# Kernel tuning notes

Measured on AMD Instinct MI355X. Metric: run time of the kernel, lower is better.

## Reference

```python
import jax, jax.numpy as jnp
import numpy as np

N, G, NPG = 8192, 128, 64        # total nodes, graphs, nodes per graph
D_IN, H, D_OUT = 128, 128, 10
DEG = 16                          # avg degree -> E = N*DEG
K = int(NPG * 0.5)                # keep_ratio = 0.5 -> topk per graph


def setup_inputs() -> dict:
    key = jax.random.key(0)
    ks = jax.random.split(key, 20)
    E = N * DEG
    # within-graph random edges (graphs are contiguous blocks of NPG nodes)
    src = jax.random.randint(ks[0], (E,), 0, NPG)
    dst = jax.random.randint(ks[1], (E,), 0, NPG)
    offs = jnp.repeat(jnp.arange(G, dtype=jnp.int32) * NPG, NPG * DEG)
    edge_index = jnp.stack([src.astype(jnp.int32) + offs, dst.astype(jnp.int32) + offs])
    batch = jnp.repeat(jnp.arange(G, dtype=jnp.int32), NPG)
    x = jax.random.normal(ks[2], (N, D_IN), jnp.float32)

    def lin(k, i, o):
        return jax.random.normal(k, (i, o), jnp.float32) * (1.0 / np.sqrt(i))

    return {
        "x": x, "edge_index": edge_index, "batch": batch,
        "W1": lin(ks[3], D_IN, H), "b1": jnp.zeros((H,), jnp.float32),
        "W2": lin(ks[4], H, H),    "b2": jnp.zeros((H,), jnp.float32),
        "W3": lin(ks[5], H, H),    "b3": jnp.zeros((H,), jnp.float32),
        "Wa": lin(ks[6], 3 * H, 1), "ba": jnp.zeros((1,), jnp.float32),
        "M1": lin(ks[7], 6 * H, H),      "c1": jnp.zeros((H,), jnp.float32),
        "M2": lin(ks[8], H, H // 2),     "c2": jnp.zeros((H // 2,), jnp.float32),
        "M3": lin(ks[9], H // 2, D_OUT), "c3": jnp.zeros((D_OUT,), jnp.float32),
    }


def reference(x, edge_index, batch, W1, b1, W2, b2, W3, b3, Wa, ba,
              M1, c1, M2, c2, M3, c3):
    n = x.shape[0]
    # generate_adjacency: dense [N,N] from edge list (symmetrized)
    A = jnp.zeros((n, n), x.dtype).at[edge_index[0], edge_index[1]].set(1.0)
    A = jnp.maximum(A, A.T)
    # normalize_adjacency: D^{-1/2} (A + I) D^{-1/2}
    A = A + jnp.eye(n, dtype=x.dtype)
    dinv = jax.lax.rsqrt(A.sum(axis=1))
    A = A * dinv[:, None] * dinv[None, :]

    gcn = lambda X, W, b: A @ (X @ W) + b
    h1 = jax.nn.relu(gcn(x, W1, b1))
    h2 = jax.nn.relu(gcn(h1, W2, b2))
    h3 = jax.nn.relu(gcn(h2, W3, b3))
    feats = jnp.concatenate([h1, h2, h3], axis=1)          # [N, 3H]

    # SelfAttentionPooling: GCN attention score + tanh + per-graph topk
    score = jnp.tanh((A @ (feats @ Wa) + ba)[:, 0])        # [N]
    s = score.reshape(G, NPG)                              # [G, NPG]
    _, idx = jax.lax.top_k(s, K)                           # [G, K]
    fg = feats.reshape(G, NPG, 3 * H)
    sel = jnp.take_along_axis(fg, idx[..., None], axis=1)  # [G, K, 3H]
    ssel = jnp.take_along_axis(s, idx, axis=1)             # [G, K]
    masked = sel * ssel[..., None]

    # Readout: mean || max per graph -> [G, 6H]
    readout = jnp.concatenate([masked.mean(axis=1), masked.max(axis=1)], axis=1)

    # MLP (dropout inactive at inference)
    h = jax.nn.relu(readout @ M1 + c1)
    h = jax.nn.relu(h @ M2 + c2)
    return h @ M3 + c3                                     # [G, D_OUT]
```

## Files before the change

### kernel.cpp

```cpp
#include <hip/hip_runtime.h>


#define NGRAPH 128
#define EPG    1024
#define ETOT   131072
#define DIM    128
#define KSEL   32
#define SA     68
#define SF     132

#define O_A    0
#define O_B0   4352
#define O_T    12800
#define O_PPAR 21248
#define O_PRE  22272
#define O_SC   22336
#define O_SEL  22400
#define LDS_FLOATS 22464
#define LDS_BYTES  (LDS_FLOATS * 4)
#define O_RO   O_T
#define O_MH   (O_T + 768)
#define O_HM   (O_T + 1792)
#define O_H2M  (O_T + 1920)

#define FMA8(A, xs, w0, w1) do { \
  A[0] += (xs)*(w0).x; A[1] += (xs)*(w0).y; A[2] += (xs)*(w0).z; A[3] += (xs)*(w0).w; \
  A[4] += (xs)*(w1).x; A[5] += (xs)*(w1).y; A[6] += (xs)*(w1).z; A[7] += (xs)*(w1).w; } while(0)

__device__ void gcn_layer(float* lds, const float* __restrict__ Wg,
                          const float* __restrict__ bg,
                          const float* __restrict__ waCol,
                          float* __restrict__ Hg, int tid)
{
  float* sA   = lds + O_A;
  float* B0   = lds + O_B0;
  float* sT   = lds + O_T;
  float* ppar = lds + O_PPAR;
  float* pre  = lds + O_PRE;
  const int r  = tid & 63;
  const int w  = tid >> 6;
  const int c0 = __builtin_amdgcn_readfirstlane(w * 8);

  float acc[8] = {0.f,0.f,0.f,0.f,0.f,0.f,0.f,0.f};
  const float* wp = Wg + c0;
  #pragma unroll 2
  for (int kq = 0; kq < 32; ++kq) {
    float4 xv = *(const float4*)&B0[r * SF + kq * 4];
    const float* wr = wp + (kq * 4) * DIM;
    float4 w00 = *(const float4*)&wr[0];
    float4 w01 = *(const float4*)&wr[4];
    float4 w10 = *(const float4*)&wr[DIM];
    float4 w11 = *(const float4*)&wr[DIM + 4];
    float4 w20 = *(const float4*)&wr[2 * DIM];
    float4 w21 = *(const float4*)&wr[2 * DIM + 4];
    float4 w30 = *(const float4*)&wr[3 * DIM];
    float4 w31 = *(const float4*)&wr[3 * DIM + 4];
    FMA8(acc, xv.x, w00, w01);
    FMA8(acc, xv.y, w10, w11);
    FMA8(acc, xv.z, w20, w21);
    FMA8(acc, xv.w, w30, w31);
  }
  *(float4*)&sT[r * SF + c0]     = make_float4(acc[0], acc[1], acc[2], acc[3]);
  *(float4*)&sT[r * SF + c0 + 4] = make_float4(acc[4], acc[5], acc[6], acc[7]);
  __syncthreads();

  float4 bv0 = *(const float4*)&bg[c0];
  float4 bv1 = *(const float4*)&bg[c0 + 4];
  float a2[8];
  a2[0] = bv0.x; a2[1] = bv0.y; a2[2] = bv0.z; a2[3] = bv0.w;
  a2[4] = bv1.x; a2[5] = bv1.y; a2[6] = bv1.z; a2[7] = bv1.w;
  #pragma unroll 4
  for (int jq = 0; jq < 16; ++jq) {
    float4 a4 = *(const float4*)&sA[r * SA + jq * 4];
    const float* tb = sT + (jq * 4) * SF + c0;
    float4 t0, t1;
    t0 = *(const float4*)&tb[0];      t1 = *(const float4*)&tb[4];
    FMA8(a2, a4.x, t0, t1);
    t0 = *(const float4*)&tb[SF];     t1 = *(const float4*)&tb[SF + 4];
    FMA8(a2, a4.y, t0, t1);
    t0 = *(const float4*)&tb[2 * SF]; t1 = *(const float4*)&tb[2 * SF + 4];
    FMA8(a2, a4.z, t0, t1);
    t0 = *(const float4*)&tb[3 * SF]; t1 = *(const float4*)&tb[3 * SF + 4];
    FMA8(a2, a4.w, t0, t1);
  }
  float4 o0, o1;
  o0.x = fmaxf(a2[0], 0.f); o0.y = fmaxf(a2[1], 0.f);
  o0.z = fmaxf(a2[2], 0.f); o0.w = fmaxf(a2[3], 0.f);
  o1.x = fmaxf(a2[4], 0.f); o1.y = fmaxf(a2[5], 0.f);
  o1.z = fmaxf(a2[6], 0.f); o1.w = fmaxf(a2[7], 0.f);
  *(float4*)&B0[r * SF + c0]      = o0;
  *(float4*)&B0[r * SF + c0 + 4]  = o1;
  *(float4*)&Hg[r * DIM + c0]     = o0;
  *(float4*)&Hg[r * DIM + c0 + 4] = o1;
  float4 wa0 = *(const float4*)&waCol[c0];
  float4 wa1 = *(const float4*)&waCol[c0 + 4];
  ppar[w * 64 + r] = o0.x*wa0.x + o0.y*wa0.y + o0.z*wa0.z + o0.w*wa0.w
                   + o1.x*wa1.x + o1.y*wa1.y + o1.z*wa1.z + o1.w*wa1.w;
  __syncthreads();
  if (tid < 64) {
    float s = 0.f;
    #pragma unroll
    for (int q = 0; q < 16; ++q) s += ppar[q * 64 + tid];
    pre[tid] += s;
  }
  __syncthreads();
}

extern "C" __global__ void __launch_bounds__(1024)
sagpool(const float* __restrict__ x,  const int* __restrict__ ei,
        const float* __restrict__ W1, const float* __restrict__ b1,
        const float* __restrict__ W2, const float* __restrict__ b2,
        const float* __restrict__ W3, const float* __restrict__ b3,
        const float* __restrict__ Wa, const float* __restrict__ ba,
        const float* __restrict__ M1, const float* __restrict__ c1,
        const float* __restrict__ M2, const float* __restrict__ c2,
        const float* __restrict__ M3, const float* __restrict__ c3,
        float* __restrict__ h1w, float* __restrict__ h2w,
        float* __restrict__ h3w, float* __restrict__ out)
{
  extern __shared__ float lds[];
  const int g = blockIdx.x, tid = threadIdx.x;
  float* sA  = lds + O_A;
  float* B0  = lds + O_B0;
  float* pre = lds + O_PRE;
  float* sc  = lds + O_SC;
  float* sel = lds + O_SEL;
  float* ro  = lds + O_RO;
  float* mh  = lds + O_MH;
  float* hm  = lds + O_HM;
  float* h2m = lds + O_H2M;

  for (int i = tid; i < 64 * SA; i += 1024) sA[i] = 0.f;
  if (tid < 64) pre[tid] = 0.f;
  __syncthreads();
  {
    int s = ei[g * EPG + tid] & 63;
    int d = ei[ETOT + g * EPG + tid] & 63;
    sA[s * SA + d] = 1.0f;
    sA[d * SA + s] = 1.0f;
  }
  __syncthreads();
  if (tid < 64) sA[tid * SA + tid] += 1.0f;
  __syncthreads();
  {
    int r = tid >> 4, q = tid & 15;
    float sum = sA[r * SA + q * 4]     + sA[r * SA + q * 4 + 1]
              + sA[r * SA + q * 4 + 2] + sA[r * SA + q * 4 + 3];
    sum += __shfl_xor(sum, 1);
    sum += __shfl_xor(sum, 2);
    sum += __shfl_xor(sum, 4);
    sum += __shfl_xor(sum, 8);
    if (q == 0) sc[r] = 1.0f / sqrtf(sum);
  }
  __syncthreads();
  for (int i = tid; i < 4096; i += 1024) {
    int r = i >> 6, c = i & 63;
    sA[r * SA + c] *= sc[r] * sc[c];
  }
  {
    const float4* xg = (const float4*)(x + g * 64 * DIM);
    for (int i = tid; i < 2048; i += 1024) {
      int r = i >> 5, q = i & 31;
      *(float4*)&B0[r * SF + q * 4] = xg[i];
    }
  }
  __syncthreads();

  gcn_layer(lds, W1, b1, Wa,           h1w + g * 8192, tid);
  gcn_layer(lds, W2, b2, Wa + DIM,     h2w + g * 8192, tid);
  gcn_layer(lds, W3, b3, Wa + 2 * DIM, h3w + g * 8192, tid);

  {
    int r = tid >> 4, q = tid & 15;
    float p = sA[r * SA + q * 4]     * pre[q * 4]
            + sA[r * SA + q * 4 + 1] * pre[q * 4 + 1]
            + sA[r * SA + q * 4 + 2] * pre[q * 4 + 2]
            + sA[r * SA + q * 4 + 3] * pre[q * 4 + 3];
    p += __shfl_xor(p, 1);
    p += __shfl_xor(p, 2);
    p += __shfl_xor(p, 4);
    p += __shfl_xor(p, 8);
    if (q == 0) sc[r] = tanhf(p + ba[0]);
  }
  __syncthreads();

  if (tid < 64) {
    float mys = sc[tid];
    int cnt = 0;
    for (int j = 0; j < 64; ++j) {
      float sj = sc[j];
      cnt += (sj > mys || (sj == mys && j < tid)) ? 1 : 0;
    }
    sel[tid] = (cnt < KSEL) ? 1.0f : 0.0f;
  }
  __syncthreads();

  if (tid < 768) {
    int c = tid >> 1, half = tid & 1;
    int which = c >> 7, cc = c & 127;
    const float* hb = ((which == 0) ? h1w : (which == 1) ? h2w : h3w) + g * 8192;
    float sum = 0.f, mx = -1e30f;
    for (int i = half * 32; i < half * 32 + 32; ++i) {
      if (sel[i] > 0.5f) {
        float v = sc[i] * hb[i * DIM + cc];
        sum += v;
        mx = fmaxf(mx, v);
      }
    }
    sum += __shfl_xor(sum, 1);
    mx = fmaxf(mx, __shfl_xor(mx, 1));
    if (half == 0) {
      ro[c]       = sum * (1.0f / KSEL);
      ro[384 + c] = mx;
    }
  }
  __syncthreads();

  {
    int j = tid & 127, oc = tid >> 7;
    float a = 0.f;
    int k0 = oc * 96;
    for (int k = k0; k < k0 + 96; k += 4) {
      float4 r4 = *(const float4*)&ro[k];
      a += r4.x * M1[(k + 0) * DIM + j];
      a += r4.y * M1[(k + 1) * DIM + j];
      a += r4.z * M1[(k + 2) * DIM + j];
      a += r4.w * M1[(k + 3) * DIM + j];
    }
    mh[oc * 128 + j] = a;
  }
  __syncthreads();
  if (tid < 128) {
    float v = c1[tid];
    #pragma unroll
    for (int q = 0; q < 8; ++q) v += mh[q * 128 + tid];
    hm[tid] = fmaxf(v, 0.f);
  }
  __syncthreads();
  if (tid < 64) {
    float a = c2[tid];
    for (int k = 0; k < 128; ++k) a += hm[k] * M2[k * 64 + tid];
    h2m[tid] = fmaxf(a, 0.f);
  }
  __syncthreads();
  if (tid < 10) {
    float a = c3[tid];
    for (int k = 0; k < 64; ++k) a += h2m[k] * M3[k * 10 + tid];
    out[g * 10 + tid] = a;
  }
}

extern "C" void kernel_launch(void* const* d_in, const int* in_sizes, int n_in,
                              void* d_out, int out_size, void* d_ws, size_t ws_size,
                              hipStream_t stream) {
  const float* x  = (const float*)d_in[0];
  const int*   ei = (const int*)d_in[1];
  const float* W1 = (const float*)d_in[3];
  const float* b1 = (const float*)d_in[4];
  const float* W2 = (const float*)d_in[5];
  const float* b2 = (const float*)d_in[6];
  const float* W3 = (const float*)d_in[7];
  const float* b3 = (const float*)d_in[8];
  const float* Wa = (const float*)d_in[9];
  const float* ba = (const float*)d_in[10];
  const float* M1 = (const float*)d_in[11];
  const float* c1 = (const float*)d_in[12];
  const float* M2 = (const float*)d_in[13];
  const float* c2 = (const float*)d_in[14];
  const float* M3 = (const float*)d_in[15];
  const float* c3 = (const float*)d_in[16];
  float* out = (float*)d_out;

  float* ws  = (float*)d_ws;
  float* h1w = ws;
  float* h2w = ws + 1048576;
  float* h3w = ws + 2097152;

  (void)hipFuncSetAttribute(reinterpret_cast<const void*>(sagpool),
                            hipFuncAttributeMaxDynamicSharedMemorySize, LDS_BYTES);
  sagpool<<<NGRAPH, 1024, LDS_BYTES, stream>>>(x, ei, W1, b1, W2, b2, W3, b3,
                                               Wa, ba, M1, c1, M2, c2, M3, c3,
                                               h1w, h2w, h3w, out);
}
```

Measured before the change: 146.8 us.

## Broadcast XW via wave readlane instead of LDS staging; ping-pong feature buffers

Inside each GCN layer, each wave keeps its 64x8 slice of X@W in registers and performs the A@(XW) product by broadcasting lanes with readlane, instead of writing XW to LDS and synchronising. Input and output feature buffers now alternate between two LDS regions, so the in-layer __syncthreads and the LDS round trip for T are removed. The cost is 512 scalar readlane operations per thread per layer, which are serial SALU/VALU work, in place of vectorized LDS reads.

```diff
diff --git a/kernel.cpp b/kernel.cpp
--- a/kernel.cpp
+++ b/kernel.cpp
@@ -11,30 +11,33 @@
 
 #define O_A    0
 #define O_B0   4352
-#define O_T    12800
+#define O_B1   12800
 #define O_PPAR 21248
 #define O_PRE  22272
 #define O_SC   22336
 #define O_SEL  22400
 #define LDS_FLOATS 22464
 #define LDS_BYTES  (LDS_FLOATS * 4)
-#define O_RO   O_T
-#define O_MH   (O_T + 768)
-#define O_HM   (O_T + 1792)
-#define O_H2M  (O_T + 1920)
+#define O_RO   O_B0
+#define O_MH   (O_B0 + 768)
+#define O_HM   (O_B0 + 1792)
+#define O_H2M  (O_B0 + 1920)
 
 #define FMA8(A, xs, w0, w1) do { \
   A[0] += (xs)*(w0).x; A[1] += (xs)*(w0).y; A[2] += (xs)*(w0).z; A[3] += (xs)*(w0).w; \
   A[4] += (xs)*(w1).x; A[5] += (xs)*(w1).y; A[6] += (xs)*(w1).z; A[7] += (xs)*(w1).w; } while(0)
 
-__device__ void gcn_layer(float* lds, const float* __restrict__ Wg,
+__device__ __forceinline__ float rdlane(float v, int lane) {
+  return __int_as_float(__builtin_amdgcn_readlane(__float_as_int(v), lane));
+}
+
+__device__ void gcn_layer(float* lds, const float* Bin, float* Bout,
+                          const float* __restrict__ Wg,
                           const float* __restrict__ bg,
                           const float* __restrict__ waCol,
                           float* __restrict__ Hg, int tid)
 {
   float* sA   = lds + O_A;
-  float* B0   = lds + O_B0;
-  float* sT   = lds + O_T;
   float* ppar = lds + O_PPAR;
   float* pre  = lds + O_PRE;
   const int r  = tid & 63;
@@ -45,7 +48,7 @@
   const float* wp = Wg + c0;
   #pragma unroll 2
   for (int kq = 0; kq < 32; ++kq) {
-    float4 xv = *(const float4*)&B0[r * SF + kq * 4];
+    float4 xv = *(const float4*)&Bin[r * SF + kq * 4];
     const float* wr = wp + (kq * 4) * DIM;
     float4 w00 = *(const float4*)&wr[0];
     float4 w01 = *(const float4*)&wr[4];
@@ -60,38 +63,33 @@
     FMA8(acc, xv.z, w20, w21);
     FMA8(acc, xv.w, w30, w31);
   }
-  *(float4*)&sT[r * SF + c0]     = make_float4(acc[0], acc[1], acc[2], acc[3]);
-  *(float4*)&sT[r * SF + c0 + 4] = make_float4(acc[4], acc[5], acc[6], acc[7]);
-  __syncthreads();
 
   float4 bv0 = *(const float4*)&bg[c0];
   float4 bv1 = *(const float4*)&bg[c0 + 4];
-  float a2[8];
-  a2[0] = bv0.x; a2[1] = bv0.y; a2[2] = bv0.z; a2[3] = bv0.w;
-  a2[4] = bv1.x; a2[5] = bv1.y; a2[6] = bv1.z; a2[7] = bv1.w;
-  #pragma unroll 4
+  float h[8];
+  h[0] = bv0.x; h[1] = bv0.y; h[2] = bv0.z; h[3] = bv0.w;
+  h[4] = bv1.x; h[5] = bv1.y; h[6] = bv1.z; h[7] = bv1.w;
   for (int jq = 0; jq < 16; ++jq) {
     float4 a4 = *(const float4*)&sA[r * SA + jq * 4];
-    const float* tb = sT + (jq * 4) * SF + c0;
-    float4 t0, t1;
-    t0 = *(const float4*)&tb[0];      t1 = *(const float4*)&tb[4];
-    FMA8(a2, a4.x, t0, t1);
-    t0 = *(const float4*)&tb[SF];     t1 = *(const float4*)&tb[SF + 4];
-    FMA8(a2, a4.y, t0, t1);
-    t0 = *(const float4*)&tb[2 * SF]; t1 = *(const float4*)&tb[2 * SF + 4];
-    FMA8(a2, a4.z, t0, t1);
-    t0 = *(const float4*)&tb[3 * SF]; t1 = *(const float4*)&tb[3 * SF + 4];
-    FMA8(a2, a4.w, t0, t1);
+    #pragma unroll
+    for (int jj = 0; jj < 4; ++jj) {
+      const int lane = jq * 4 + jj;
+      const float aj = (jj == 0) ? a4.x : (jj == 1) ? a4.y
+                     : (jj == 2) ? a4.z : a4.w;
+      #pragma unroll
+      for (int c = 0; c < 8; ++c)
+        h[c] += aj * rdlane(acc[c], lane);
+    }
   }
   float4 o0, o1;
-  o0.x = fmaxf(a2[0], 0.f); o0.y = fmaxf(a2[1], 0.f);
-  o0.z = fmaxf(a2[2], 0.f); o0.w = fmaxf(a2[3], 0.f);
-  o1.x = fmaxf(a2[4], 0.f); o1.y = fmaxf(a2[5], 0.f);
-  o1.z = fmaxf(a2[6], 0.f); o1.w = fmaxf(a2[7], 0.f);
-  *(float4*)&B0[r * SF + c0]      = o0;
-  *(float4*)&B0[r * SF + c0 + 4]  = o1;
-  *(float4*)&Hg[r * DIM + c0]     = o0;
-  *(float4*)&Hg[r * DIM + c0 + 4] = o1;
+  o0.x = fmaxf(h[0], 0.f); o0.y = fmaxf(h[1], 0.f);
+  o0.z = fmaxf(h[2], 0.f); o0.w = fmaxf(h[3], 0.f);
+  o1.x = fmaxf(h[4], 0.f); o1.y = fmaxf(h[5], 0.f);
+  o1.z = fmaxf(h[6], 0.f); o1.w = fmaxf(h[7], 0.f);
+  *(float4*)&Bout[r * SF + c0]     = o0;
+  *(float4*)&Bout[r * SF + c0 + 4] = o1;
+  *(float4*)&Hg[r * DIM + c0]      = o0;
+  *(float4*)&Hg[r * DIM + c0 + 4]  = o1;
   float4 wa0 = *(const float4*)&waCol[c0];
   float4 wa1 = *(const float4*)&waCol[c0 + 4];
   ppar[w * 64 + r] = o0.x*wa0.x + o0.y*wa0.y + o0.z*wa0.z + o0.w*wa0.w
@@ -122,6 +120,7 @@
   const int g = blockIdx.x, tid = threadIdx.x;
   float* sA  = lds + O_A;
   float* B0  = lds + O_B0;
+  float* B1  = lds + O_B1;
   float* pre = lds + O_PRE;
   float* sc  = lds + O_SC;
   float* sel = lds + O_SEL;
@@ -166,9 +165,9 @@
   }
   __syncthreads();
 
-  gcn_layer(lds, W1, b1, Wa,           h1w + g * 8192, tid);
-  gcn_layer(lds, W2, b2, Wa + DIM,     h2w + g * 8192, tid);
-  gcn_layer(lds, W3, b3, Wa + 2 * DIM, h3w + g * 8192, tid);
+  gcn_layer(lds, B0, B1, W1, b1, Wa,           h1w + g * 8192, tid);
+  gcn_layer(lds, B1, B0, W2, b2, Wa + DIM,     h2w + g * 8192, tid);
+  gcn_layer(lds, B0, B1, W3, b3, Wa + 2 * DIM, h3w + g * 8192, tid);
 
   {
     int r = tid >> 4, q = tid & 15;
```

New measurement: 154.6 us. 1.05x slower.
